# Performance work log

Hardware: AMD Instinct MI355X
Metric: run time of the kernel (lower is better)

Reference implementation:

```python
import jax, jax.numpy as jnp
import numpy as np


def setup_inputs() -> dict:
    key = jax.random.key(0)
    k1, k2, k3, k4 = jax.random.split(key, 4)
    B, T, C, H = 4, 4096, 1024, 64
    x = jax.random.normal(k1, (B, T, C), dtype=jnp.float32)
    # nn.Linear weights, stored as (in, out) for x @ W
    s = 1.0 / np.sqrt(C)
    Wk = jax.random.uniform(k2, (C, H), dtype=jnp.float32, minval=-s, maxval=s)
    Wq = jax.random.uniform(k3, (C, H), dtype=jnp.float32, minval=-s, maxval=s)
    Wv = jax.random.uniform(k4, (C, H), dtype=jnp.float32, minval=-s, maxval=s)
    return {"x": x, "Wk": Wk, "Wq": Wq, "Wv": Wv}


def reference(x, Wk, Wq, Wv):
    # single-head causal self-attention (dropout=0 / eval mode)
    B, T, C = x.shape
    k = x @ Wk  # [B,T,H]
    q = x @ Wq  # [B,T,H]
    v = x @ Wv  # [B,T,H]
    scale = k.shape[-1] ** -0.5
    wei = jnp.einsum('bth,bsh->bts', q, k) * scale  # [B,T,T]
    causal = jnp.tril(jnp.ones((T, T), dtype=bool))
    wei = jnp.where(causal, wei, -jnp.inf)
    wei = jax.nn.softmax(wei, axis=-1)
    out = jnp.einsum('bts,bsh->bth', wei, v)  # [B,T,H]
    return out
```

## Files before the change

### kernel.cpp

```cpp
#include <hip/hip_runtime.h>
#include <hip/hip_bf16.h>

#define B_ 4
#define T_ 4096
#define C_ 1024
#define H_ 64
#define M_ (B_ * T_)
#define UPB 272

typedef __bf16 bf16x8 __attribute__((ext_vector_type(8)));
typedef float f32x8 __attribute__((ext_vector_type(8)));
typedef float f32x4 __attribute__((ext_vector_type(4)));
typedef unsigned short us8 __attribute__((ext_vector_type(8)));
typedef unsigned short us4 __attribute__((ext_vector_type(4)));

#define QSCALE 0.18033688011112042f
#define OFF2   23.083120654223414f

__device__ __forceinline__ unsigned short f2bf(float x) {
    return __builtin_bit_cast(unsigned short, (__bf16)x);
}
__device__ __forceinline__ float bf2f(unsigned short u) {
    return __builtin_bit_cast(float, (unsigned)u << 16);
}
__device__ __forceinline__ f32x4 mfma16(bf16x8 a, bf16x8 b, f32x4 c) {
    return __builtin_amdgcn_mfma_f32_16x16x32_bf16(a, b, c, 0, 0, 0);
}
__device__ __forceinline__ bf16x8 ldb8(const unsigned short* p) {
    return __builtin_bit_cast(bf16x8, *reinterpret_cast<const us8*>(p));
}
__device__ __forceinline__ bf16x8 ldlds8(const char* p) {
    return __builtin_bit_cast(bf16x8, *reinterpret_cast<const us8*>(p));
}
__device__ __forceinline__ void gll16(const void* g, char* ldsdst) {
    __builtin_amdgcn_global_load_lds(
        (const __attribute__((address_space(1))) unsigned*)g,
        (__attribute__((address_space(3))) unsigned*)ldsdst, 16, 0, 0);
}

__global__ __launch_bounds__(256) void wt_kernel(const float* __restrict__ Wk,
                                                 const float* __restrict__ Wq,
                                                 const float* __restrict__ Wv,
                                                 unsigned short* __restrict__ Wt) {
    __shared__ float t[64][65];
    const int wid = blockIdx.x >> 4;
    const int kb = (blockIdx.x & 15) * 64;
    const float* W = (wid == 0) ? Wk : (wid == 1 ? Wq : Wv);
    const int ty = threadIdx.x >> 6;
    const int tx = threadIdx.x & 63;
#pragma unroll
    for (int i = 0; i < 16; ++i) {
        int kl = i * 4 + ty;
        t[kl][tx] = W[(size_t)(kb + kl) * H_ + tx];
    }
    __syncthreads();
#pragma unroll
    for (int i = 0; i < 16; ++i) {
        int hl = i * 4 + ty;
        Wt[(size_t)(wid * 64 + hl) * C_ + kb + tx] = f2bf(t[tx][hl]);
    }
}

__global__ __launch_bounds__(256) void proj_kernel(const float* __restrict__ x,
                                                   const unsigned short* __restrict__ Wt,
                                                   unsigned short* __restrict__ Kb,
                                                   unsigned short* __restrict__ Qb,
                                                   unsigned short* __restrict__ Vt) {
    __shared__ char lds[61440];
    const int tid = threadIdx.x;
    const int w = tid >> 6, l = tid & 63;
    const int lg = l >> 4, cl = l & 15;
    const int mbase = blockIdx.x * 64;
    const int w64 = w << 6;

    f32x4 acc[12];
#pragma unroll
    for (int i = 0; i < 12; ++i) acc[i] = (f32x4){0.f, 0.f, 0.f, 0.f};

#define STAGE(AO, BO, KC)                                                        \
    {                                                                            \
        _Pragma("unroll") for (int i = 0; i < 2; ++i) {                          \
            int unit = i * 256 + tid;                                            \
            int row = unit >> 3, up = unit & 7;                                  \
            int lu = up ^ (row & 7);                                             \
            gll16(x + (size_t)(mbase + row) * C_ + (KC) + lu * 4,                \
                  lds + (AO) + (unsigned)(i * 256 + w64) * 16);                  \
        }                                                                        \
        _Pragma("unroll") for (int i = 0; i < 3; ++i) {                          \
            int unit = i * 256 + tid;                                            \
            int pr = unit >> 3, up = unit & 7;                                   \
            int u = up ^ (pr & 7);                                               \
            int r = pr * 2 + (u >> 2);                                           \
            gll16(Wt + (size_t)r * C_ + (KC) + (u & 3) * 8,                      \
                  lds + (BO) + (unsigned)(i * 256 + w64) * 16);                  \
        }                                                                        \
    }

#define COMPUTE(AO, BO)                                                          \
    {                                                                            \
        const int arow = w * 16 + cl;                                            \
        const int asw = cl & 7;                                                  \
        f32x4 alo = *reinterpret_cast<const f32x4*>(                             \
            lds + (AO) + arow * 128 + ((lg * 2) ^ asw) * 16);                    \
        f32x4 ahi = *reinterpret_cast<const f32x4*>(                             \
            lds + (AO) + arow * 128 + ((lg * 2 + 1) ^ asw) * 16);                \
        f32x8 af;                                                                \
        af[0] = alo[0]; af[1] = alo[1]; af[2] = alo[2]; af[3] = alo[3];          \
        af[4] = ahi[0]; af[5] = ahi[1]; af[6] = ahi[2]; af[7] = ahi[3];          \
        bf16x8 a = __builtin_convertvector(af, bf16x8);                          \
        _Pragma("unroll") for (int nf = 0; nf < 12; ++nf) {                      \
            int r = nf * 16 + cl;                                                \
            int pr = r >> 1;                                                     \
            bf16x8 bb = __builtin_bit_cast(bf16x8,                               \
                *reinterpret_cast<const us8*>(                                   \
                    lds + (BO) + pr * 128 +                                      \
                    ((((cl & 1) << 2) + lg) ^ (pr & 7)) * 16));                  \
            acc[nf] = mfma16(a, bb, acc[nf]);                                    \
        }                                                                        \
    }

    int a0 = 0, a1 = 8192, a2 = 16384;
    int b0 = 24576, b1 = 36864, b2 = 49152;

    STAGE(a0, b0, 0);
    STAGE(a1, b1, 32);
    for (int t = 0; t < 30; ++t) {
        asm volatile("s_waitcnt vmcnt(5)" ::: "memory");
        asm volatile("s_barrier" ::: "memory");
        STAGE(a2, b2, (t + 2) * 32);
        COMPUTE(a0, b0);
        int ta = a0; a0 = a1; a1 = a2; a2 = ta;
        int tb = b0; b0 = b1; b1 = b2; b2 = tb;
    }
    asm volatile("s_waitcnt vmcnt(5)" ::: "memory");
    asm volatile("s_barrier" ::: "memory");
    COMPUTE(a0, b0);
    asm volatile("s_waitcnt vmcnt(0)" ::: "memory");
    asm volatile("s_barrier" ::: "memory");
    COMPUTE(a1, b1);
#undef STAGE
#undef COMPUTE

    const int rbase = mbase + w * 16 + lg * 4;
#pragma unroll
    for (int nf = 0; nf < 12; ++nf) {
        int colg = nf * 16 + cl;
#pragma unroll
        for (int r = 0; r < 4; ++r) {
            float v = acc[nf][r];
            int m = rbase + r;
            if (colg < 64) {
                Kb[m * H_ + colg] = f2bf(v);
            } else if (colg < 128) {
                Qb[m * H_ + (colg - 64)] = f2bf(v * QSCALE);
            } else {
                int b = m >> 12, t = m & 4095, h = colg - 128;
                Vt[((b << 6) + h) * T_ + t] = f2bf(v);
            }
        }
    }
}

__global__ __launch_bounds__(256, 2) void attn_kernel(const unsigned short* __restrict__ Qb,
                                                      const unsigned short* __restrict__ Kb,
                                                      const unsigned short* __restrict__ Vt,
                                                      float* __restrict__ out,
                                                      unsigned short* __restrict__ Opart,
                                                      float* __restrict__ lpart) {
    __shared__ char lds[49152];
    const int tid = threadIdx.x;
    const int w = tid >> 6, l = tid & 63;
    const int lg = l >> 4, cl = l & 15;
    const int kgrp = lg * 8;
    char* pb = lds + 32768 + w * 4096;

    const int lin = blockIdx.x;
    const int xcd = lin & 7;
    const int b = xcd >> 1;
    const int f = (xcd & 1) * 136 + (lin >> 3);

    int qt = 0, Sp = 0;
    while (f >= Sp + ((qt + 2) >> 1)) { Sp += (qt + 2) >> 1; ++qt; }
    const int chunk = f - Sp;
    const int nc = (qt + 2) >> 1;

    const int qbase = qt * 128;
    const int qw = qbase + w * 32;
    const int s0 = chunk * 256;
    int s1 = s0 + 256;
    if (s1 > qbase + 128) s1 = qbase + 128;
    const int ntile = (s1 - s0) >> 6;

    const unsigned short* q0 = Qb + (size_t)(b * T_ + qw + cl) * H_;
    bf16x8 qa00 = ldb8(q0 + kgrp), qa01 = ldb8(q0 + 32 + kgrp);
    bf16x8 qa10 = ldb8(q0 + 16 * H_ + kgrp), qa11 = ldb8(q0 + 16 * H_ + 32 + kgrp);

    f32x4 o[2][4];
#pragma unroll
    for (int rf = 0; rf < 2; ++rf)
#pragma unroll
        for (int nf = 0; nf < 4; ++nf) o[rf][nf] = (f32x4){0.f, 0.f, 0.f, 0.f};
    float lrow[2][4] = {{0.f, 0.f, 0.f, 0.f}, {0.f, 0.f, 0.f, 0.f}};

#define STG(KO, VO, SB)                                                          \
    {                                                                            \
        _Pragma("unroll") for (int i = 0; i < 2; ++i) {                          \
            int u = i * 256 + tid;                                               \
            int row = u >> 3, up = u & 7;                                        \
            int lu = up ^ (row & 7);                                             \
            gll16(Kb + (size_t)(b * T_ + (SB) + row) * H_ + lu * 8,              \
                  lds + (KO) + (unsigned)(i * 256 + (w << 6)) * 16);             \
            gll16(Vt + (size_t)((b << 6) + row) * T_ + (SB) + lu * 8,            \
                  lds + (VO) + (unsigned)(i * 256 + (w << 6)) * 16);             \
        }                                                                        \
    }

    int k0o = 0, k1o = 8192;
    int v0o = 16384, v1o = 24576;

    STG(k0o, v0o, s0);
    for (int t = 0; t < ntile; ++t) {
        const int sbase = s0 + t * 64;
        asm volatile("s_waitcnt vmcnt(0)" ::: "memory");
        asm volatile("s_barrier" ::: "memory");
        if (t + 1 < ntile) STG(k1o, v1o, sbase + 64);

        if (qw + 31 >= sbase) {
            f32x4 sA[4], sB[4];
            __builtin_amdgcn_s_setprio(1);
#pragma unroll
            for (int nf = 0; nf < 4; ++nf) {
                const int row = nf * 16 + cl, sw = row & 7;
                bf16x8 k0v = ldlds8(lds + k0o + row * 128 + (lg ^ sw) * 16);
                bf16x8 k1v = ldlds8(lds + k0o + row * 128 + ((4 + lg) ^ sw) * 16);
                f32x4 z = (f32x4){0.f, 0.f, 0.f, 0.f};
                sA[nf] = mfma16(qa01, k1v, mfma16(qa00, k0v, z));
                sB[nf] = mfma16(qa11, k1v, mfma16(qa10, k0v, z));
            }
            __builtin_amdgcn_s_setprio(0);
            if (sbase + 63 > qw) {
#pragma unroll
                for (int nf = 0; nf < 4; ++nf) {
                    const int col = sbase + nf * 16 + cl;
#pragma unroll
                    for (int r = 0; r < 4; ++r) {
                        const int rowA = qw + lg * 4 + r;
                        if (col > rowA)      sA[nf][r] = -1e30f;
                        if (col > rowA + 16) sB[nf][r] = -1e30f;
                    }
                }
            }
#pragma unroll
            for (int nf = 0; nf < 4; ++nf) {
#pragma unroll
                for (int r = 0; r < 4; ++r) {
                    const int row = lg * 4 + r;
                    float pA = exp2f(sA[nf][r] - OFF2);
                    float pB = exp2f(sB[nf][r] - OFF2);
                    lrow[0][r] += pA;
                    lrow[1][r] += pB;
                    const int swz = (row & 7) << 4;
                    int lin0 = row * 128 + (nf * 16 + cl) * 2;
                    int lin1 = (16 + row) * 128 + (nf * 16 + cl) * 2;
                    *(unsigned short*)(pb + (lin0 ^ swz)) = f2bf(pA);
                    *(unsigned short*)(pb + (lin1 ^ swz)) = f2bf(pB);
                }
            }
            const int msk = (cl & 7) << 4;
            bf16x8 pa00 = ldlds8(pb + ((cl * 128 + lg * 16) ^ msk));
            bf16x8 pa01 = ldlds8(pb + ((cl * 128 + 64 + lg * 16) ^ msk));
            bf16x8 pa10 = ldlds8(pb + (((16 + cl) * 128 + lg * 16) ^ msk));
            bf16x8 pa11 = ldlds8(pb + (((16 + cl) * 128 + 64 + lg * 16) ^ msk));
            __builtin_amdgcn_s_setprio(1);
#pragma unroll
            for (int nf = 0; nf < 4; ++nf) {
                const int row = nf * 16 + cl, sw = row & 7;
                bf16x8 v0 = ldlds8(lds + v0o + row * 128 + (lg ^ sw) * 16);
                bf16x8 v1 = ldlds8(lds + v0o + row * 128 + ((4 + lg) ^ sw) * 16);
                o[0][nf] = mfma16(pa01, v1, mfma16(pa00, v0, o[0][nf]));
                o[1][nf] = mfma16(pa11, v1, mfma16(pa10, v0, o[1][nf]));
            }
            __builtin_amdgcn_s_setprio(0);
        }
        int tk = k0o; k0o = k1o; k1o = tk;
        int tv = v0o; v0o = v1o; v1o = tv;
    }
#undef STG

#pragma unroll
    for (int o16 = 1; o16 < 16; o16 <<= 1)
#pragma unroll
        for (int rf = 0; rf < 2; ++rf)
#pragma unroll
            for (int r = 0; r < 4; ++r)
                lrow[rf][r] += __shfl_xor(lrow[rf][r], o16);

    if (nc == 1) {
#pragma unroll
        for (int rf = 0; rf < 2; ++rf) {
            float inv[4];
#pragma unroll
            for (int r = 0; r < 4; ++r) inv[r] = 1.0f / lrow[rf][r];
#pragma unroll
            for (int nf = 0; nf < 4; ++nf)
#pragma unroll
                for (int r = 0; r < 4; ++r) {
                    int t = qw + rf * 16 + lg * 4 + r;
                    out[(size_t)(b * T_ + t) * H_ + nf * 16 + cl] =
                        o[rf][nf][r] * inv[r];
                }
        }
    } else {
        const int slot = b * UPB + f;
        unsigned short* Ob = Opart + (size_t)slot * 8192;
#pragma unroll
        for (int rf = 0; rf < 2; ++rf)
#pragma unroll
            for (int nf = 0; nf < 4; ++nf) {
                us4 v;
#pragma unroll
                for (int r = 0; r < 4; ++r) v[r] = f2bf(o[rf][nf][r]);
                *reinterpret_cast<us4*>(Ob + ((w * 8 + rf * 4 + nf) * 64 + l) * 4) = v;
            }
        if (cl == 0) {
#pragma unroll
            for (int rf = 0; rf < 2; ++rf)
#pragma unroll
                for (int r = 0; r < 4; ++r)
                    lpart[slot * 128 + w * 32 + rf * 16 + lg * 4 + r] = lrow[rf][r];
        }
    }
}

__global__ __launch_bounds__(256) void combine_kernel(const unsigned short* __restrict__ Opart,
                                                      const float* __restrict__ lpart,
                                                      float* __restrict__ out) {
    const int qt = 2 + blockIdx.x;
    const int b = blockIdx.y;
    const int c = (qt + 2) >> 1;
    const int slot0 = b * UPB + ((qt + 1) * (qt + 1)) / 4;

    const int p = blockIdx.z * 4 + (threadIdx.x >> 6);
    const int l = threadIdx.x & 63;
    const int wq = p >> 3, rf = (p >> 2) & 1, nf = p & 3;
    const int lg = l >> 4, cl = l & 15;

    float a[4] = {0.f, 0.f, 0.f, 0.f};
    float ls[4] = {0.f, 0.f, 0.f, 0.f};
    for (int j = 0; j < c; ++j) {
        const unsigned short* src =
            Opart + (size_t)(slot0 + j) * 8192 + (p * 64 + l) * 4;
        us4 v = *reinterpret_cast<const us4*>(src);
        const float* lp = lpart + (slot0 + j) * 128 + wq * 32 + rf * 16 + lg * 4;
#pragma unroll
        for (int e = 0; e < 4; ++e) {
            a[e] += bf2f(v[e]);
            ls[e] += lp[e];
        }
    }
#pragma unroll
    for (int e = 0; e < 4; ++e) {
        int row = qt * 128 + wq * 32 + rf * 16 + lg * 4 + e;
        out[(size_t)(b * T_ + row) * H_ + nf * 16 + cl] = a[e] / ls[e];
    }
}

extern "C" void kernel_launch(void* const* d_in, const int* in_sizes, int n_in,
                              void* d_out, int out_size, void* d_ws, size_t ws_size,
                              hipStream_t stream) {
    const float* x  = (const float*)d_in[0];
    const float* Wk = (const float*)d_in[1];
    const float* Wq = (const float*)d_in[2];
    const float* Wv = (const float*)d_in[3];
    float* out = (float*)d_out;

    char* ws = (char*)d_ws;
    unsigned short* Kb = (unsigned short*)(ws);
    unsigned short* Qb = (unsigned short*)(ws + 2097152);
    unsigned short* Vt = (unsigned short*)(ws + 2 * 2097152);
    unsigned short* Wt = (unsigned short*)(ws + 3 * 2097152);
    const size_t base = 6684672ull;
    unsigned short* Opart = (unsigned short*)(ws + base);
    float* lpart = (float*)(ws + base + (size_t)B_ * UPB * 16384);

    wt_kernel<<<dim3(48), dim3(256), 0, stream>>>(Wk, Wq, Wv, Wt);
    proj_kernel<<<dim3(256), dim3(256), 0, stream>>>(x, Wt, Kb, Qb, Vt);
    attn_kernel<<<dim3(8 * 136), dim3(256), 0, stream>>>(
        Qb, Kb, Vt, out, Opart, lpart);
    combine_kernel<<<dim3(30, B_, 8), dim3(256), 0, stream>>>(Opart, lpart, out);
}
```

Measured before the change: 59.58 us.

## Stage K/V tiles through registers into single LDS buffer

```diff
diff --git a/kernel.cpp b/kernel.cpp
--- a/kernel.cpp
+++ b/kernel.cpp
@@ -161,18 +161,18 @@
     }
 }
 
-__global__ __launch_bounds__(256, 2) void attn_kernel(const unsigned short* __restrict__ Qb,
-                                                      const unsigned short* __restrict__ Kb,
-                                                      const unsigned short* __restrict__ Vt,
-                                                      float* __restrict__ out,
-                                                      unsigned short* __restrict__ Opart,
-                                                      float* __restrict__ lpart) {
-    __shared__ char lds[49152];
+__global__ __launch_bounds__(256) void attn_kernel(const unsigned short* __restrict__ Qb,
+                                                   const unsigned short* __restrict__ Kb,
+                                                   const unsigned short* __restrict__ Vt,
+                                                   float* __restrict__ out,
+                                                   unsigned short* __restrict__ Opart,
+                                                   float* __restrict__ lpart) {
+    __shared__ char lds[32768];
     const int tid = threadIdx.x;
     const int w = tid >> 6, l = tid & 63;
     const int lg = l >> 4, cl = l & 15;
     const int kgrp = lg * 8;
-    char* pb = lds + 32768 + w * 4096;
+    char* pb = lds + 16384 + w * 4096;
 
     const int lin = blockIdx.x;
     const int xcd = lin & 7;
@@ -202,28 +202,32 @@
         for (int nf = 0; nf < 4; ++nf) o[rf][nf] = (f32x4){0.f, 0.f, 0.f, 0.f};
     float lrow[2][4] = {{0.f, 0.f, 0.f, 0.f}, {0.f, 0.f, 0.f, 0.f}};
 
-#define STG(KO, VO, SB)                                                          \
+    const int u0 = tid,        r0 = u0 >> 3, lu0 = (u0 & 7) ^ (r0 & 7);
+    const int u1 = 256 + tid,  r1 = u1 >> 3, lu1 = (u1 & 7) ^ (r1 & 7);
+    us8 kr0, kr1, vr0, vr1;
+#define LDREG(SB)                                                                \
     {                                                                            \
-        _Pragma("unroll") for (int i = 0; i < 2; ++i) {                          \
-            int u = i * 256 + tid;                                               \
-            int row = u >> 3, up = u & 7;                                        \
-            int lu = up ^ (row & 7);                                             \
-            gll16(Kb + (size_t)(b * T_ + (SB) + row) * H_ + lu * 8,              \
-                  lds + (KO) + (unsigned)(i * 256 + (w << 6)) * 16);             \
-            gll16(Vt + (size_t)((b << 6) + row) * T_ + (SB) + lu * 8,            \
-                  lds + (VO) + (unsigned)(i * 256 + (w << 6)) * 16);             \
-        }                                                                        \
-    }
-
-    int k0o = 0, k1o = 8192;
-    int v0o = 16384, v1o = 24576;
-
-    STG(k0o, v0o, s0);
+        kr0 = *reinterpret_cast<const us8*>(                                     \
+            Kb + (size_t)(b * T_ + (SB) + r0) * H_ + lu0 * 8);                   \
+        kr1 = *reinterpret_cast<const us8*>(                                     \
+            Kb + (size_t)(b * T_ + (SB) + r1) * H_ + lu1 * 8);                   \
+        vr0 = *reinterpret_cast<const us8*>(                                     \
+            Vt + (size_t)((b << 6) + r0) * T_ + (SB) + lu0 * 8);                 \
+        vr1 = *reinterpret_cast<const us8*>(                                     \
+            Vt + (size_t)((b << 6) + r1) * T_ + (SB) + lu1 * 8);                 \
+    }
+
+    LDREG(s0);
     for (int t = 0; t < ntile; ++t) {
         const int sbase = s0 + t * 64;
-        asm volatile("s_waitcnt vmcnt(0)" ::: "memory");
         asm volatile("s_barrier" ::: "memory");
-        if (t + 1 < ntile) STG(k1o, v1o, sbase + 64);
+        *reinterpret_cast<us8*>(lds + u0 * 16) = kr0;
+        *reinterpret_cast<us8*>(lds + u1 * 16) = kr1;
+        *reinterpret_cast<us8*>(lds + 8192 + u0 * 16) = vr0;
+        *reinterpret_cast<us8*>(lds + 8192 + u1 * 16) = vr1;
+        if (t + 1 < ntile) LDREG(sbase + 64);
+        asm volatile("s_waitcnt lgkmcnt(0)" ::: "memory");
+        asm volatile("s_barrier" ::: "memory");
 
         if (qw + 31 >= sbase) {
             f32x4 sA[4], sB[4];
@@ -231,8 +235,8 @@
 #pragma unroll
             for (int nf = 0; nf < 4; ++nf) {
                 const int row = nf * 16 + cl, sw = row & 7;
-                bf16x8 k0v = ldlds8(lds + k0o + row * 128 + (lg ^ sw) * 16);
-                bf16x8 k1v = ldlds8(lds + k0o + row * 128 + ((4 + lg) ^ sw) * 16);
+                bf16x8 k0v = ldlds8(lds + row * 128 + (lg ^ sw) * 16);
+                bf16x8 k1v = ldlds8(lds + row * 128 + ((4 + lg) ^ sw) * 16);
                 f32x4 z = (f32x4){0.f, 0.f, 0.f, 0.f};
                 sA[nf] = mfma16(qa01, k1v, mfma16(qa00, k0v, z));
                 sB[nf] = mfma16(qa11, k1v, mfma16(qa10, k0v, z));
@@ -275,17 +279,15 @@
 #pragma unroll
             for (int nf = 0; nf < 4; ++nf) {
                 const int row = nf * 16 + cl, sw = row & 7;
-                bf16x8 v0 = ldlds8(lds + v0o + row * 128 + (lg ^ sw) * 16);
-                bf16x8 v1 = ldlds8(lds + v0o + row * 128 + ((4 + lg) ^ sw) * 16);
+                bf16x8 v0 = ldlds8(lds + 8192 + row * 128 + (lg ^ sw) * 16);
+                bf16x8 v1 = ldlds8(lds + 8192 + row * 128 + ((4 + lg) ^ sw) * 16);
                 o[0][nf] = mfma16(pa01, v1, mfma16(pa00, v0, o[0][nf]));
                 o[1][nf] = mfma16(pa11, v1, mfma16(pa10, v0, o[1][nf]));
             }
             __builtin_amdgcn_s_setprio(0);
         }
-        int tk = k0o; k0o = k1o; k1o = tk;
-        int tv = v0o; v0o = v1o; v1o = tv;
-    }
-#undef STG
+    }
+#undef LDREG
 
 #pragma unroll
     for (int o16 = 1; o16 < 16; o16 <<= 1)
```

New measurement: 65.07 us. 1.09x slower.
